# Optimization experiments

Hardware: AMD Instinct MI355X
Metric: run time of the kernel (lower is better)

The kernel has to match this reference:

```python
import jax, jax.numpy as jnp
import numpy as np

B, L, D = 2, 401, 128


def setup_inputs() -> dict:
    key = jax.random.key(0)
    ks = jax.random.split(key, 9)
    s = 1.0 / np.sqrt(D)
    return {
        "x": jax.random.normal(ks[0], (B, L, D), dtype=jnp.float32),
        # nn.Bilinear weight (out=D, in1=D, in2=D) and bias (D,)
        "W_bil": jax.random.uniform(ks[1], (D, D, D), jnp.float32, -s, s),
        "b_bil": jax.random.uniform(ks[2], (D,), jnp.float32, -s, s),
        # LayerNorm(D)
        "ln_g": jnp.ones((D,), jnp.float32),
        "ln_b": jnp.zeros((D,), jnp.float32),
        # Linear(D, D)
        "W1": jax.random.uniform(ks[3], (D, D), jnp.float32, -s, s),
        "b1": jax.random.uniform(ks[4], (D,), jnp.float32, -s, s),
        # Linear(D, 1)
        "w2": jax.random.uniform(ks[5], (D,), jnp.float32, -s, s),
        "b2": jax.random.uniform(ks[6], (1,), jnp.float32, -s, s),
    }


def reference(x, W_bil, b_bil, ln_g, ln_b, W1, b1, w2, b2):
    # Bilinear: pair[b,i,j,k] = x[b,i,:] @ W_bil[k] @ x[b,j,:] + b_bil[k]
    # Contract in two steps to avoid an O(L^2 D^2) intermediate:
    tmp = jnp.einsum('bid,kde->bike', x, W_bil)          # (B,L,D,D)
    pair = jnp.einsum('bike,bje->bijk', tmp, x) + b_bil  # (B,L,L,D)
    # LayerNorm over D
    mu = jnp.mean(pair, axis=-1, keepdims=True)
    var = jnp.mean(jnp.square(pair - mu), axis=-1, keepdims=True)
    h = (pair - mu) * jax.lax.rsqrt(var + 1e-5) * ln_g + ln_b
    # Linear -> GELU (exact, torch default) -> Dropout(eval: identity) -> Linear(D,1)
    h = jax.nn.gelu(jnp.einsum('bijd,ed->bije', h, W1) + b1, approximate=False)
    contact = jnp.einsum('bijd,d->bij', h, w2) + b2[0]   # (B,L,L)
    return 0.5 * (contact + jnp.swapaxes(contact, 1, 2))
```

## Files before the change

kernel.cpp:

```cpp
#include <hip/hip_runtime.h>
#include <hip/hip_bf16.h>

#define L 401
#define D 128
#define BATCH 2
#define PADU 136
#define PADB 272

typedef __attribute__((ext_vector_type(8))) short short8;
typedef __attribute__((ext_vector_type(4))) float f32x4;

__device__ __forceinline__ ushort bf16_bits(float f) {
  __hip_bfloat16 h = __float2bfloat16(f);
  return *reinterpret_cast<ushort*>(&h);
}

__device__ __forceinline__ float gelu_fast(float v) {
  const float a = fabsf(v) * 0.70710678118654752f;
  const float t = __builtin_amdgcn_rcpf(fmaf(a, 0.47047f, 1.0f));
  float p = fmaf(t, 0.3739278f, -0.0479399f);
  p = fmaf(p, t, 0.1740121f);
  p = p * t;
  const float e = __builtin_amdgcn_exp2f(a * a * -1.4426950408889634f);
  const float q = p * e;
  const float cdf = (v < 0.f) ? q : 1.0f - q;
  return v * cdf;
}

__device__ __forceinline__ short8 frag_read_swz(const char* lds, int row, int cb) {
  return *(const short8*)(lds + row * 256 + (cb ^ ((row & 7) << 4)));
}

__device__ __forceinline__ void stage_swz(char* lds, const __hip_bfloat16* src,
                                          int row0, int rowmax, int tid) {
#pragma unroll
  for (int it = 0; it < 4; ++it) {
    int r = it * 32 + (tid >> 4);
    int cb = (tid & 15) * 16;
    int sr = row0 + r;
    sr = sr > rowmax ? rowmax : sr;
    short8 v = *(const short8*)((const char*)src + (size_t)sr * 256 + cb);
    *(short8*)(lds + r * 256 + (cb ^ ((r & 7) << 4))) = v;
  }
}

__device__ __forceinline__ void stage_pad(char* lds, const __hip_bfloat16* src,
                                          int row0, int rowmax, int tid) {
#pragma unroll
  for (int it = 0; it < 4; ++it) {
    int r = it * 32 + (tid >> 4);
    int cb = (tid & 15) * 16;
    int sr = row0 + r;
    sr = sr > rowmax ? rowmax : sr;
    short8 v = *(const short8*)((const char*)src + (size_t)sr * 256 + cb);
    *(short8*)(lds + r * PADB + cb) = v;
  }
}

__global__ void prep_kernel(const float* __restrict__ x, const float* __restrict__ W_bil,
                            const float* __restrict__ W1, const float* __restrict__ ln_g,
                            const float* __restrict__ ln_b, const float* __restrict__ b1,
                            __hip_bfloat16* __restrict__ xbf, __hip_bfloat16* __restrict__ wbt,
                            __hip_bfloat16* __restrict__ wgbf, float* __restrict__ s1,
                            float* __restrict__ s2b1) {
  __shared__ alignas(16) ushort t[128 * PADU];
  __shared__ float red[8];
  const int bid = blockIdx.x;
  const int tid = threadIdx.x;
  if (bid < 128) {
    const float* in = W_bil + (size_t)bid * D * D;
#pragma unroll
    for (int it = 0; it < 16; ++it) {
      int idx = it * 256 + tid;
      int d = idx >> 5;
      int m = idx & 31;
      int e = m * 4;
      int swz = (m & 15) << 3;
      float4 f4 = ((const float4*)in)[idx];
      char* base = (char*)t;
      *(ushort*)(base + (size_t)(e + 0) * PADB + ((2 * d) ^ swz)) = bf16_bits(f4.x);
      *(ushort*)(base + (size_t)(e + 1) * PADB + ((2 * d) ^ swz)) = bf16_bits(f4.y);
      *(ushort*)(base + (size_t)(e + 2) * PADB + ((2 * d) ^ swz)) = bf16_bits(f4.z);
      *(ushort*)(base + (size_t)(e + 3) * PADB + ((2 * d) ^ swz)) = bf16_bits(f4.w);
    }
    __syncthreads();
    ushort* out = (ushort*)(wbt + (size_t)bid * D * D);
    const int e = tid >> 1;
    const int dh = (tid & 1) * 64;
    const int swz = ((e >> 2) & 15) << 3;
    const char* base = (const char*)t + (size_t)e * PADB;
#pragma unroll
    for (int c = 0; c < 16; ++c) {
      int d0 = dh + c * 4;
      unsigned long long v = *(const unsigned long long*)(base + ((2 * d0) ^ swz));
      *(unsigned long long*)&out[e * D + d0] = v;
    }
  } else if (bid < 154) {
    const int n4 = (BATCH * L * D) / 4;
    int i4 = (bid - 128) * 1024 + tid;
#pragma unroll
    for (int c = 0; c < 4; ++c) {
      int idx = i4 + c * 256;
      if (idx < n4) {
        float4 f4 = ((const float4*)x)[idx];
        ushort4 o;
        o.x = bf16_bits(f4.x); o.y = bf16_bits(f4.y);
        o.z = bf16_bits(f4.z); o.w = bf16_bits(f4.w);
        ((ushort4*)xbf)[idx] = o;
      }
    }
  } else {
    const int e = bid - 154;
    float s1p = 0.f, s2p = 0.f;
    if (tid < 128) {
      const int d = tid;
      const float wv = W1[e * D + d];
      const float wg = wv * ln_g[d];
      wgbf[e * D + d] = __float2bfloat16(wg);
      s1p = wg;
      s2p = wv * ln_b[d];
    }
#pragma unroll
    for (int m = 1; m <= 32; m <<= 1) {
      s1p += __shfl_xor(s1p, m);
      s2p += __shfl_xor(s2p, m);
    }
    const int wv_ = tid >> 6;
    if ((tid & 63) == 0) { red[wv_ * 2] = s1p; red[wv_ * 2 + 1] = s2p; }
    __syncthreads();
    if (tid == 0) {
      s1[e] = red[0] + red[2] + red[4] + red[6];
      s2b1[e] = red[1] + red[3] + red[5] + red[7] + b1[e];
    }
  }
}

__global__ __launch_bounds__(512, 4) void gemm_tmp(const __hip_bfloat16* __restrict__ xbf,
                                                   const __hip_bfloat16* __restrict__ wbt,
                                                   __hip_bfloat16* __restrict__ tmp) {
  __shared__ char ldsE[128 * 256];
  __shared__ char ldsI[128 * 256];
  const int tid = threadIdx.x;
  const int lane = tid & 63;
  const int w = tid >> 6;
  const int c0 = lane & 15;
  const int lg = lane >> 4;
  const int kt = blockIdx.x;
  const int i0 = blockIdx.y * 128;
  const int b = blockIdx.z;

  stage_swz(ldsI, xbf + (size_t)b * L * D, i0, L - 1, tid);
  stage_swz(ldsE, wbt + (size_t)kt * D * D, 0, 127, tid);
  __syncthreads();

  f32x4 acc[8];
#pragma unroll
  for (int cf = 0; cf < 8; ++cf) acc[cf] = (f32x4){0.f, 0.f, 0.f, 0.f};

#pragma unroll
  for (int ks = 0; ks < 4; ++ks) {
    const int cb = ks * 64 + lg * 16;
    short8 ae = frag_read_swz(ldsE, w * 16 + c0, cb);
#pragma unroll
    for (int cf = 0; cf < 8; ++cf) {
      short8 bi = frag_read_swz(ldsI, cf * 16 + c0, cb);
      acc[cf] = __builtin_amdgcn_mfma_f32_16x16x32_bf16(ae, bi, acc[cf], 0, 0, 0);
    }
  }

  ushort* outp = (ushort*)tmp;
  const int e0 = w * 16 + lg * 4;
#pragma unroll
  for (int cf = 0; cf < 8; ++cf) {
    const int i = i0 + cf * 16 + c0;
    if (i < L) {
      uint lo = (uint)bf16_bits(acc[cf][0]) | ((uint)bf16_bits(acc[cf][1]) << 16);
      uint hi = (uint)bf16_bits(acc[cf][2]) | ((uint)bf16_bits(acc[cf][3]) << 16);
      uint2 v; v.x = lo; v.y = hi;
      *(uint2*)(outp + ((size_t)(b * L + i)) * (D * D) + kt * D + e0) = v;
    }
  }
}

__global__ __launch_bounds__(512, 4) void fused_contact(
    const __hip_bfloat16* __restrict__ xbf, const __hip_bfloat16* __restrict__ tmp,
    const __hip_bfloat16* __restrict__ wgbf, const float* __restrict__ b_bil,
    const float* __restrict__ s1, const float* __restrict__ s2b1,
    const float* __restrict__ w2, const float* __restrict__ b2,
    float* __restrict__ cont) {
  __shared__ char ldsX[128 * PADB];
  __shared__ char ldsT[128 * PADB];
  const int tid = threadIdx.x;
  const int lane = tid & 63;
  const int w = tid >> 6;
  const int c0 = lane & 15;
  const int lg = lane >> 4;
  const int b = blockIdx.z;
  const int i = blockIdx.y;
  const int j0 = blockIdx.x * 128;
  const bool live = (j0 + w * 16) < L;

  stage_pad(ldsX, xbf + (size_t)b * L * D, j0, L - 1, tid);
  stage_pad(ldsT, tmp + ((size_t)(b * L + i)) * (D * D), 0, 127, tid);
  __syncthreads();

  const int aBase = (w * 16 + c0) * PADB + lg * 16;
  const int bBase = c0 * PADB + lg * 16;

  f32x4 acc[8];
  float rs[4], nm[4];
  if (live) {
#pragma unroll
    for (int cf = 0; cf < 8; ++cf) acc[cf] = (f32x4){0.f, 0.f, 0.f, 0.f};
#pragma unroll
    for (int ks = 0; ks < 4; ++ks) {
      short8 a0 = *(const short8*)(ldsX + aBase + ks * 64);
#pragma unroll
      for (int cf = 0; cf < 8; ++cf) {
        short8 bb = *(const short8*)(ldsT + bBase + cf * (16 * PADB) + ks * 64);
        acc[cf] = __builtin_amdgcn_mfma_f32_16x16x32_bf16(a0, bb, acc[cf], 0, 0, 0);
      }
    }
#pragma unroll
    for (int cf = 0; cf < 8; ++cf) {
      const float bbia = b_bil[cf * 16 + c0];
#pragma unroll
      for (int r = 0; r < 4; ++r) acc[cf][r] += bbia;
    }
#pragma unroll
    for (int r = 0; r < 4; ++r) {
      float s = 0.f, q = 0.f;
#pragma unroll
      for (int cf = 0; cf < 8; ++cf) {
        float v = acc[cf][r];
        s += v;
        q += v * v;
      }
      s += __shfl_xor(s, 1); s += __shfl_xor(s, 2); s += __shfl_xor(s, 4); s += __shfl_xor(s, 8);
      q += __shfl_xor(q, 1); q += __shfl_xor(q, 2); q += __shfl_xor(q, 4); q += __shfl_xor(q, 8);
      const float m = s * (1.f / 128.f);
      const float var = q * (1.f / 128.f) - m * m;
      rs[r] = __builtin_amdgcn_rsqf(var + 1e-5f);
      nm[r] = -rs[r] * m;
    }
  }
  __syncthreads();

  if (live) {
#pragma unroll
    for (int cf = 0; cf < 8; ++cf)
#pragma unroll
      for (int r = 0; r < 4; ++r)
        *(ushort*)(ldsX + (w * 16 + lg * 4 + r) * PADB + (cf * 16 + c0) * 2) =
            bf16_bits(acc[cf][r]);
  }
  stage_pad(ldsT, wgbf, 0, 127, tid);
  __syncthreads();
  if (!live) return;

  f32x4 acc2[8];
#pragma unroll
  for (int cf = 0; cf < 8; ++cf) acc2[cf] = (f32x4){0.f, 0.f, 0.f, 0.f};
#pragma unroll
  for (int ks = 0; ks < 4; ++ks) {
    short8 a0 = *(const short8*)(ldsX + aBase + ks * 64);
#pragma unroll
    for (int cf = 0; cf < 8; ++cf) {
      short8 bb = *(const short8*)(ldsT + bBase + cf * (16 * PADB) + ks * 64);
      acc2[cf] = __builtin_amdgcn_mfma_f32_16x16x32_bf16(a0, bb, acc2[cf], 0, 0, 0);
    }
  }

  float s1v[8], c2v[8], w2v[8];
#pragma unroll
  for (int cf = 0; cf < 8; ++cf) {
    const int c = cf * 16 + c0;
    s1v[cf] = s1[c];
    c2v[cf] = s2b1[c];
    w2v[cf] = w2[c];
  }
  const float b2v = b2[0];
  float part[4] = {0.f, 0.f, 0.f, 0.f};
#pragma unroll
  for (int cf = 0; cf < 8; ++cf)
#pragma unroll
    for (int r = 0; r < 4; ++r) {
      const float v = fmaf(acc2[cf][r], rs[r], fmaf(nm[r], s1v[cf], c2v[cf]));
      part[r] += gelu_fast(v) * w2v[cf];
    }
#pragma unroll
  for (int r = 0; r < 4; ++r) {
    float p = part[r];
    p += __shfl_xor(p, 1); p += __shfl_xor(p, 2); p += __shfl_xor(p, 4); p += __shfl_xor(p, 8);
    if (c0 == 0) {
      const int j = j0 + w * 16 + lg * 4 + r;
      if (j < L) cont[((size_t)(b * L + i)) * L + j] = p + b2v;
    }
  }
}

__global__ void sym_kernel(const float* __restrict__ c, float* __restrict__ out) {
  int idx = blockIdx.x * 256 + threadIdx.x;
  const int n = BATCH * L * L;
  if (idx >= n) return;
  int b = idx / (L * L);
  int r = idx - b * (L * L);
  int i = r / L;
  int j = r - i * L;
  out[idx] = 0.5f * (c[(size_t)b * L * L + (size_t)i * L + j] +
                     c[(size_t)b * L * L + (size_t)j * L + i]);
}

extern "C" void kernel_launch(void* const* d_in, const int* in_sizes, int n_in,
                              void* d_out, int out_size, void* d_ws, size_t ws_size,
                              hipStream_t stream) {
  const float* x     = (const float*)d_in[0];
  const float* W_bil = (const float*)d_in[1];
  const float* b_bil = (const float*)d_in[2];
  const float* ln_g  = (const float*)d_in[3];
  const float* ln_b  = (const float*)d_in[4];
  const float* W1    = (const float*)d_in[5];
  const float* b1    = (const float*)d_in[6];
  const float* w2    = (const float*)d_in[7];
  const float* b2    = (const float*)d_in[8];
  float* out = (float*)d_out;

  char* ws = (char*)d_ws;
  __hip_bfloat16* xbf  = (__hip_bfloat16*)(ws + 0);
  __hip_bfloat16* wgbf = (__hip_bfloat16*)(ws + 205312);
  float* s1            = (float*)(ws + 238080);
  float* s2b1          = (float*)(ws + 238592);
  __hip_bfloat16* wbt  = (__hip_bfloat16*)(ws + 239104);
  __hip_bfloat16* tmp  = (__hip_bfloat16*)(ws + 4433408);
  float* cont          = (float*)(ws + 30713344);

  prep_kernel<<<282, 256, 0, stream>>>(x, W_bil, W1, ln_g, ln_b, b1,
                                       xbf, wbt, wgbf, s1, s2b1);
  gemm_tmp<<<dim3(D, 4, BATCH), 512, 0, stream>>>(xbf, wbt, tmp);
  fused_contact<<<dim3(4, L, BATCH), 512, 0, stream>>>(xbf, tmp, wgbf, b_bil,
                                                       s1, s2b1, w2, b2, cont);
  sym_kernel<<<(BATCH * L * L + 255) / 256, 256, 0, stream>>>(cont, out);
}
```

Before: 172.4 us.

## Swap MFMA operand roles so each lane owns one j row; prefetch W1 to registers

The two MFMA stages now put the weight or tmp tile in the A operand and the x row in the B operand. The output fragment is transposed, so each lane column holds a single j position. This cuts the LayerNorm and final reductions to two cross-lane shuffles on one scalar. It also allows packed 8-byte bf16 stores to LDS instead of scalar 2-byte ones, and vectorized float4 parameter loads. The W1 tile is loaded from global memory into registers before the first barrier, so that latency overlaps the first GEMM, at the cost of extra registers under a 512x4 launch bound.

```diff
diff --git a/kernel.cpp b/kernel.cpp
--- a/kernel.cpp
+++ b/kernel.cpp
@@ -198,104 +198,116 @@
   const int b = blockIdx.z;
   const int i = blockIdx.y;
   const int j0 = blockIdx.x * 128;
+  const int jme = j0 + w * 16 + c0;
   const bool live = (j0 + w * 16) < L;
 
   stage_pad(ldsX, xbf + (size_t)b * L * D, j0, L - 1, tid);
   stage_pad(ldsT, tmp + ((size_t)(b * L + i)) * (D * D), 0, 127, tid);
+
+  short8 wgreg[4];
+  {
+    const char* wsrc = (const char*)wgbf;
+    const int cb = (tid & 15) * 16;
+#pragma unroll
+    for (int it = 0; it < 4; ++it) {
+      int r = it * 32 + (tid >> 4);
+      wgreg[it] = *(const short8*)(wsrc + (size_t)r * 256 + cb);
+    }
+  }
   __syncthreads();
 
-  const int aBase = (w * 16 + c0) * PADB + lg * 16;
-  const int bBase = c0 * PADB + lg * 16;
-
-  f32x4 acc[8];
-  float rs[4], nm[4];
+  const int ownBase = (w * 16 + c0) * PADB;
+  float rs = 0.f, nm = 0.f;
+
   if (live) {
-#pragma unroll
-    for (int cf = 0; cf < 8; ++cf) acc[cf] = (f32x4){0.f, 0.f, 0.f, 0.f};
+    f32x4 acc1[8];
+#pragma unroll
+    for (int kf = 0; kf < 8; ++kf) acc1[kf] = (f32x4){0.f, 0.f, 0.f, 0.f};
+
 #pragma unroll
     for (int ks = 0; ks < 4; ++ks) {
-      short8 a0 = *(const short8*)(ldsX + aBase + ks * 64);
-#pragma unroll
-      for (int cf = 0; cf < 8; ++cf) {
-        short8 bb = *(const short8*)(ldsT + bBase + cf * (16 * PADB) + ks * 64);
-        acc[cf] = __builtin_amdgcn_mfma_f32_16x16x32_bf16(a0, bb, acc[cf], 0, 0, 0);
+      short8 bx = *(const short8*)(ldsX + ownBase + lg * 16 + ks * 64);
+#pragma unroll
+      for (int kf = 0; kf < 8; ++kf) {
+        short8 at = *(const short8*)(ldsT + (kf * 16 + c0) * PADB + lg * 16 + ks * 64);
+        acc1[kf] = __builtin_amdgcn_mfma_f32_16x16x32_bf16(at, bx, acc1[kf], 0, 0, 0);
       }
     }
-#pragma unroll
-    for (int cf = 0; cf < 8; ++cf) {
-      const float bbia = b_bil[cf * 16 + c0];
-#pragma unroll
-      for (int r = 0; r < 4; ++r) acc[cf][r] += bbia;
-    }
-#pragma unroll
-    for (int r = 0; r < 4; ++r) {
-      float s = 0.f, q = 0.f;
-#pragma unroll
-      for (int cf = 0; cf < 8; ++cf) {
-        float v = acc[cf][r];
+
+    float s = 0.f, q = 0.f;
+#pragma unroll
+    for (int kf = 0; kf < 8; ++kf) {
+      const float4 bb = *(const float4*)&b_bil[kf * 16 + lg * 4];
+      acc1[kf][0] += bb.x; acc1[kf][1] += bb.y;
+      acc1[kf][2] += bb.z; acc1[kf][3] += bb.w;
+#pragma unroll
+      for (int r = 0; r < 4; ++r) {
+        const float v = acc1[kf][r];
         s += v;
         q += v * v;
       }
-      s += __shfl_xor(s, 1); s += __shfl_xor(s, 2); s += __shfl_xor(s, 4); s += __shfl_xor(s, 8);
-      q += __shfl_xor(q, 1); q += __shfl_xor(q, 2); q += __shfl_xor(q, 4); q += __shfl_xor(q, 8);
-      const float m = s * (1.f / 128.f);
-      const float var = q * (1.f / 128.f) - m * m;
-      rs[r] = __builtin_amdgcn_rsqf(var + 1e-5f);
-      nm[r] = -rs[r] * m;
+    }
+    s += __shfl_xor(s, 16); s += __shfl_xor(s, 32);
+    q += __shfl_xor(q, 16); q += __shfl_xor(q, 32);
+    const float m = s * (1.f / 128.f);
+    const float var = q * (1.f / 128.f) - m * m;
+    rs = __builtin_amdgcn_rsqf(var + 1e-5f);
+    nm = -rs * m;
+
+#pragma unroll
+    for (int kf = 0; kf < 8; ++kf) {
+      uint lo = (uint)bf16_bits(acc1[kf][0]) | ((uint)bf16_bits(acc1[kf][1]) << 16);
+      uint hi = (uint)bf16_bits(acc1[kf][2]) | ((uint)bf16_bits(acc1[kf][3]) << 16);
+      uint2 v; v.x = lo; v.y = hi;
+      *(uint2*)(ldsX + ownBase + kf * 32 + lg * 8) = v;
     }
   }
   __syncthreads();
 
-  if (live) {
-#pragma unroll
-    for (int cf = 0; cf < 8; ++cf)
-#pragma unroll
-      for (int r = 0; r < 4; ++r)
-        *(ushort*)(ldsX + (w * 16 + lg * 4 + r) * PADB + (cf * 16 + c0) * 2) =
-            bf16_bits(acc[cf][r]);
-  }
-  stage_pad(ldsT, wgbf, 0, 127, tid);
+  {
+    const int cb = (tid & 15) * 16;
+#pragma unroll
+    for (int it = 0; it < 4; ++it) {
+      int r = it * 32 + (tid >> 4);
+      *(short8*)(ldsT + r * PADB + cb) = wgreg[it];
+    }
+  }
   __syncthreads();
   if (!live) return;
 
   f32x4 acc2[8];
 #pragma unroll
-  for (int cf = 0; cf < 8; ++cf) acc2[cf] = (f32x4){0.f, 0.f, 0.f, 0.f};
+  for (int ef = 0; ef < 8; ++ef) acc2[ef] = (f32x4){0.f, 0.f, 0.f, 0.f};
 #pragma unroll
   for (int ks = 0; ks < 4; ++ks) {
-    short8 a0 = *(const short8*)(ldsX + aBase + ks * 64);
-#pragma unroll
-    for (int cf = 0; cf < 8; ++cf) {
-      short8 bb = *(const short8*)(ldsT + bBase + cf * (16 * PADB) + ks * 64);
-      acc2[cf] = __builtin_amdgcn_mfma_f32_16x16x32_bf16(a0, bb, acc2[cf], 0, 0, 0);
-    }
-  }
-
-  float s1v[8], c2v[8], w2v[8];
-#pragma unroll
-  for (int cf = 0; cf < 8; ++cf) {
-    const int c = cf * 16 + c0;
-    s1v[cf] = s1[c];
-    c2v[cf] = s2b1[c];
-    w2v[cf] = w2[c];
-  }
-  const float b2v = b2[0];
-  float part[4] = {0.f, 0.f, 0.f, 0.f};
-#pragma unroll
-  for (int cf = 0; cf < 8; ++cf)
-#pragma unroll
-    for (int r = 0; r < 4; ++r) {
-      const float v = fmaf(acc2[cf][r], rs[r], fmaf(nm[r], s1v[cf], c2v[cf]));
-      part[r] += gelu_fast(v) * w2v[cf];
-    }
-#pragma unroll
-  for (int r = 0; r < 4; ++r) {
-    float p = part[r];
-    p += __shfl_xor(p, 1); p += __shfl_xor(p, 2); p += __shfl_xor(p, 4); p += __shfl_xor(p, 8);
-    if (c0 == 0) {
-      const int j = j0 + w * 16 + lg * 4 + r;
-      if (j < L) cont[((size_t)(b * L + i)) * L + j] = p + b2v;
-    }
+    short8 bx = *(const short8*)(ldsX + ownBase + lg * 16 + ks * 64);
+#pragma unroll
+    for (int ef = 0; ef < 8; ++ef) {
+      short8 at = *(const short8*)(ldsT + (ef * 16 + c0) * PADB + lg * 16 + ks * 64);
+      acc2[ef] = __builtin_amdgcn_mfma_f32_16x16x32_bf16(at, bx, acc2[ef], 0, 0, 0);
+    }
+  }
+
+  float part = 0.f;
+#pragma unroll
+  for (int ef = 0; ef < 8; ++ef) {
+    const int e0 = ef * 16 + lg * 4;
+    const float4 s1v = *(const float4*)&s1[e0];
+    const float4 c2v = *(const float4*)&s2b1[e0];
+    const float4 w2v = *(const float4*)&w2[e0];
+    const float v0 = fmaf(acc2[ef][0], rs, fmaf(nm, s1v.x, c2v.x));
+    const float v1 = fmaf(acc2[ef][1], rs, fmaf(nm, s1v.y, c2v.y));
+    const float v2 = fmaf(acc2[ef][2], rs, fmaf(nm, s1v.z, c2v.z));
+    const float v3 = fmaf(acc2[ef][3], rs, fmaf(nm, s1v.w, c2v.w));
+    part += gelu_fast(v0) * w2v.x;
+    part += gelu_fast(v1) * w2v.y;
+    part += gelu_fast(v2) * w2v.z;
+    part += gelu_fast(v3) * w2v.w;
+  }
+  part += __shfl_xor(part, 16);
+  part += __shfl_xor(part, 32);
+  if (lg == 0 && jme < L) {
+    cont[((size_t)(b * L + i)) * L + jme] = part + b2[0];
   }
 }
 
```

Result: faster. 167.5 us (-2.9%).
